# Kernel optimization log

Hardware: AMD Instinct MI355X
Metric: run time of the kernel (lower is better)

Reference implementation:

```python
import jax, jax.numpy as jnp
import numpy as np

NUM_HEADS = 12


def setup_inputs() -> dict:
    key = jax.random.key(0)
    k1, k2, k3, k4 = jax.random.split(key, 4)
    dim = 768
    B, N1, N2 = 8, 64, 4096  # N1 must equal head_dim = dim // num_heads
    x = jax.random.normal(k1, (B, N1, dim), dtype=jnp.float32)
    y = jax.random.normal(k2, (B, N2, dim), dtype=jnp.float32)
    # torch nn.Linear layout: [out_features, in_features]
    W_qkv = jax.random.normal(k3, (3 * dim, dim), dtype=jnp.float32) * 0.02
    W_proj = jax.random.normal(k4, (dim, dim), dtype=jnp.float32) * 0.02
    b_proj = jnp.zeros((dim,), dtype=jnp.float32)
    return {"x": x, "y": y, "W_qkv": W_qkv, "W_proj": W_proj, "b_proj": b_proj}


def _split_heads(t, H):
    # [B, N, C] -> [B, H, N, C//H]
    B, N, C = t.shape
    return t.reshape(B, N, H, C // H).transpose(0, 2, 1, 3)


def reference(x, y, W_qkv, W_proj, b_proj):
    H = NUM_HEADS
    B1, N1, C = x.shape
    B2, N2, _ = y.shape
    hd = C // H
    scale = hd ** -0.5

    # qkv projections (bias=False); take q from x, k/v from y
    qkv_x = x @ W_qkv.T                      # [B, N1, 3C]
    q = _split_heads(qkv_x[..., :C], H)      # [B, H, N1, hd]
    qkv_y = y @ W_qkv.T                      # [B, N2, 3C]
    k = _split_heads(qkv_y[..., C:2 * C], H)  # [B, H, N2, hd]
    v = _split_heads(qkv_y[..., 2 * C:], H)   # [B, H, N2, hd]

    attn = jnp.einsum('bhqd,bhkd->bhqk', q, k) * scale  # [B, H, N1, N2]
    attn = jax.nn.softmax(attn, axis=-1)
    attn_t = attn.transpose(0, 1, 3, 2)       # [B, H, N2, N1]; N1 == hd

    # non-standard elementwise combine with v (requires N1 == hd)
    out = attn_t * v                          # [B, H, N2, hd]
    out = out.transpose(0, 2, 1, 3).reshape(B2, N2, C)
    return out @ W_proj.T + b_proj
```

## Files before the change

### kernel.cpp

```cpp
#include <hip/hip_runtime.h>
#include <math.h>


typedef __attribute__((ext_vector_type(8))) short short8;
typedef __attribute__((ext_vector_type(4))) float f32x4;

__device__ __forceinline__ ushort f2bf(float x) {
  unsigned u = __float_as_uint(x);
  u += 0x7fffu + ((u >> 16) & 1u);
  return (ushort)(u >> 16);
}
__device__ __forceinline__ float bf2f(ushort h) {
  return __uint_as_float((unsigned)h << 16);
}

__device__ __forceinline__ void gl_lds16(const ushort* g, ushort* l) {
  __builtin_amdgcn_global_load_lds(
      (__attribute__((address_space(1))) void*)g,
      (__attribute__((address_space(3))) void*)l, 16, 0, 0);
}

__global__ __launch_bounds__(256) void cast_f32_bf16(
    const float* __restrict__ src, ushort* __restrict__ dst, int n) {
  int i = (blockIdx.x * 256 + threadIdx.x) * 8;
  if (i >= n) return;
  float4 a = *(const float4*)(src + i);
  float4 b = *(const float4*)(src + i + 4);
  ushort o[8] = {f2bf(a.x), f2bf(a.y), f2bf(a.z), f2bf(a.w),
                 f2bf(b.x), f2bf(b.y), f2bf(b.z), f2bf(b.w)};
  *(uint4*)(dst + i) = *(const uint4*)o;
}

template <typename CT>
__global__ __launch_bounds__(256) void gemm_bf16_nt(
    const ushort* __restrict__ A, int lda,
    const ushort* __restrict__ B, int ldb,
    CT* __restrict__ C, int ldc, int K,
    const float* __restrict__ bias,
    int m_tiles, int n_tiles, int swz)
{
  __shared__ __align__(16) ushort As[2][4096];
  __shared__ __align__(16) ushort Bs[2][4096];
  const int tid = threadIdx.x;
  int rt, ct;
  {
    int id = blockIdx.x;
    if (swz) {
      int xcd = id & 7, local = id >> 3;
      int per = n_tiles * 16;
      int grp = local / per, s = local % per;
      rt = xcd * (m_tiles >> 3) + grp * 16 + (s & 15);
      ct = s >> 4;
    } else { rt = id % m_tiles; ct = id / m_tiles; }
  }
  const int m0 = rt * 128, n0 = ct * 128;

  const int w = tid >> 6, lane = tid & 63;
  const int lm = lane & 15, quad = lane >> 4;
  const int wm = (w & 1) * 64, wn = (w >> 1) * 64;

  const int G0 = w * 64 + lane, G1 = G0 + 256;
  const int r0 = G0 >> 2, c0 = ((G0 & 3) - (r0 >> 1)) & 3;
  const int r1 = G1 >> 2, c1 = ((G1 & 3) - (r1 >> 1)) & 3;
  const ushort* Ag0 = A + (size_t)(m0 + r0) * lda + c0 * 8;
  const ushort* Ag1 = A + (size_t)(m0 + r1) * lda + c1 * 8;
  const ushort* Bg0 = B + (size_t)(n0 + r0) * ldb + c0 * 8;
  const ushort* Bg1 = B + (size_t)(n0 + r1) * ldb + c1 * 8;
  const int lds0 = w * 512, lds1 = w * 512 + 2048;

  f32x4 acc[4][4];
#pragma unroll
  for (int i = 0; i < 4; ++i)
#pragma unroll
    for (int j = 0; j < 4; ++j) acc[i][j] = (f32x4)(0.f);

  const int nk = K >> 5;
  gl_lds16(Ag0, &As[0][lds0]); gl_lds16(Ag1, &As[0][lds1]);
  gl_lds16(Bg0, &Bs[0][lds0]); gl_lds16(Bg1, &Bs[0][lds1]);

  int cur = 0;
  for (int kk = 0; kk < nk; ++kk) {
    __syncthreads();
    if (kk + 1 < nk) {
      const int k0 = (kk + 1) << 5;
      gl_lds16(Ag0 + k0, &As[cur ^ 1][lds0]); gl_lds16(Ag1 + k0, &As[cur ^ 1][lds1]);
      gl_lds16(Bg0 + k0, &Bs[cur ^ 1][lds0]); gl_lds16(Bg1 + k0, &Bs[cur ^ 1][lds1]);
    }
    const ushort* Ab = &As[cur][0];
    const ushort* Bb = &Bs[cur][0];
    short8 af[4], bf8[4];
#pragma unroll
    for (int i = 0; i < 4; ++i) {
      const int Ra = wm + i * 16 + lm;
      af[i] = *(const short8*)(const void*)(Ab + Ra * 32 + ((quad + (Ra >> 1)) & 3) * 8);
      const int Rb = wn + i * 16 + lm;
      bf8[i] = *(const short8*)(const void*)(Bb + Rb * 32 + ((quad + (Rb >> 1)) & 3) * 8);
    }
#pragma unroll
    for (int i = 0; i < 4; ++i)
#pragma unroll
      for (int j = 0; j < 4; ++j)
        acc[i][j] = __builtin_amdgcn_mfma_f32_16x16x32_bf16(af[i], bf8[j], acc[i][j], 0, 0, 0);
    cur ^= 1;
  }
  __syncthreads();

  if constexpr (sizeof(CT) == 2) {
    ushort* eb = ((ushort*)&Bs[0][0]) + w * 2048;
#pragma unroll
    for (int i = 0; i < 4; ++i) {
      ushort* ebc = eb + (i & 1) * 1024;
#pragma unroll
      for (int j = 0; j < 4; ++j)
#pragma unroll
        for (int r = 0; r < 4; ++r) {
          const int R = quad * 4 + r;
          const int gt = j * 2 + (lm >> 3);
          const int gs = (gt + R) & 7;
          ebc[R * 64 + gs * 8 + (lm & 7)] = f2bf(acc[i][j][r]);
        }
#pragma unroll
      for (int p = 0; p < 2; ++p) {
        const int R2 = (lane >> 3) + p * 8;
        const int g = lane & 7;
        const int gt2 = (g - R2) & 7;
        uint4 v = *(const uint4*)(const void*)(ebc + R2 * 64 + g * 8);
        *(uint4*)(C + (size_t)(m0 + wm + i * 16 + R2) * ldc + n0 + wn + gt2 * 8) = v;
      }
    }
  } else {
#pragma unroll
    for (int j = 0; j < 4; ++j) {
      const int col = n0 + wn + j * 16 + lm;
      const float bb = bias ? bias[col] : 0.f;
#pragma unroll
      for (int i = 0; i < 4; ++i) {
        const int row = m0 + wm + i * 16 + quad * 4;
#pragma unroll
        for (int r = 0; r < 4; ++r)
          C[(size_t)(row + r) * ldc + col] = (CT)(acc[i][j][r] + bb);
      }
    }
  }
}

__global__ __launch_bounds__(256) void attn_pass1(
    const ushort* __restrict__ Q,
    const ushort* __restrict__ KV,
    float* __restrict__ parts)
{
  const int chunk = blockIdx.x, h = blockIdx.y, b = blockIdx.z;
  const int tid = threadIdx.x;
  __shared__ __align__(16) ushort Qs[64 * 72];
  __shared__ __align__(16) ushort Ks[128 * 72];
  __shared__ float sm[4][64], ss[4][64];
#pragma unroll
  for (int p = 0; p < 2; ++p) {
    const int G = tid + 256 * p, row = G >> 3, g = G & 7;
    *(uint4*)(Qs + row * 72 + g * 8) =
        *(const uint4*)(Q + (size_t)(b * 64 + row) * 768 + h * 64 + g * 8);
  }
#pragma unroll
  for (int p = 0; p < 4; ++p) {
    const int G = tid + 256 * p, row = G >> 3, g = G & 7;
    *(uint4*)(Ks + row * 72 + g * 8) =
        *(const uint4*)(KV + (size_t)(b * 4096 + chunk * 128 + row) * 1536 + h * 64 + g * 8);
  }
  __syncthreads();

  const int w = tid >> 6, lane = tid & 63;
  const int lm = lane & 15, quad = lane >> 4;
  const int wn = w * 32;

  f32x4 acc[4][2];
#pragma unroll
  for (int i = 0; i < 4; ++i) { acc[i][0] = (f32x4)(0.f); acc[i][1] = (f32x4)(0.f); }
#pragma unroll
  for (int s = 0; s < 2; ++s) {
    short8 qf[4], kf[2];
#pragma unroll
    for (int i = 0; i < 4; ++i)
      qf[i] = *(const short8*)(const void*)(Qs + (i * 16 + lm) * 72 + s * 32 + quad * 8);
#pragma unroll
    for (int jn = 0; jn < 2; ++jn)
      kf[jn] = *(const short8*)(const void*)(Ks + (wn + jn * 16 + lm) * 72 + s * 32 + quad * 8);
#pragma unroll
    for (int i = 0; i < 4; ++i)
#pragma unroll
      for (int jn = 0; jn < 2; ++jn)
        acc[i][jn] = __builtin_amdgcn_mfma_f32_16x16x32_bf16(qf[i], kf[jn], acc[i][jn], 0, 0, 0);
  }

#pragma unroll
  for (int i = 0; i < 4; ++i)
#pragma unroll
    for (int r = 0; r < 4; ++r) {
      float v0 = acc[i][0][r] * 0.125f, v1 = acc[i][1][r] * 0.125f;
      float m = fmaxf(v0, v1);
      m = fmaxf(m, __shfl_xor(m, 1)); m = fmaxf(m, __shfl_xor(m, 2));
      m = fmaxf(m, __shfl_xor(m, 4)); m = fmaxf(m, __shfl_xor(m, 8));
      float e = __expf(v0 - m) + __expf(v1 - m);
      e += __shfl_xor(e, 1); e += __shfl_xor(e, 2);
      e += __shfl_xor(e, 4); e += __shfl_xor(e, 8);
      if (lm == 0) {
        const int j = i * 16 + quad * 4 + r;
        sm[w][j] = m; ss[w][j] = e;
      }
    }
  __syncthreads();
  if (tid < 64) {
    float g = fmaxf(fmaxf(sm[0][tid], sm[1][tid]), fmaxf(sm[2][tid], sm[3][tid]));
    float s = ss[0][tid] * __expf(sm[0][tid] - g) + ss[1][tid] * __expf(sm[1][tid] - g)
            + ss[2][tid] * __expf(sm[2][tid] - g) + ss[3][tid] * __expf(sm[3][tid] - g);
    const int bh = b * 12 + h;
    float* p = parts + ((size_t)(bh * 32 + chunk) * 64 + tid) * 2;
    p[0] = g; p[1] = s;
  }
}

__global__ void attn_combine(const float* __restrict__ parts, float* __restrict__ stats)
{
  const int bh = blockIdx.x, j = threadIdx.x;
  float pm[32], ps[32];
  float g = -1e30f;
#pragma unroll
  for (int c = 0; c < 32; ++c) {
    const float* p = parts + ((size_t)(bh * 32 + c) * 64 + j) * 2;
    pm[c] = p[0]; ps[c] = p[1];
    g = fmaxf(g, pm[c]);
  }
  float s = 0.f;
#pragma unroll
  for (int c = 0; c < 32; ++c) s += ps[c] * __expf(pm[c] - g);
  stats[(size_t)(bh * 64 + j) * 2]     = g;
  stats[(size_t)(bh * 64 + j) * 2 + 1] = 1.f / s;
}

__global__ __launch_bounds__(256) void attn_pass2(
    const ushort* __restrict__ Q, const ushort* __restrict__ KV,
    const float* __restrict__ stats, ushort* __restrict__ E)
{
  const int chunk = blockIdx.x, h = blockIdx.y, b = blockIdx.z;
  const int tid = threadIdx.x;
  __shared__ __align__(16) ushort Qs[64 * 72];
  __shared__ __align__(16) ushort Ks[128 * 72];
  __shared__ __align__(16) ushort Vs[128 * 72];
  __shared__ float st[64][2];
#pragma unroll
  for (int p = 0; p < 2; ++p) {
    const int G = tid + 256 * p, row = G >> 3, g = G & 7;
    *(uint4*)(Qs + row * 72 + g * 8) =
        *(const uint4*)(Q + (size_t)(b * 64 + row) * 768 + h * 64 + g * 8);
  }
#pragma unroll
  for (int p = 0; p < 4; ++p) {
    const int G = tid + 256 * p, row = G >> 3, g = G & 7;
    const size_t rbase = (size_t)(b * 4096 + chunk * 128 + row) * 1536 + h * 64 + g * 8;
    *(uint4*)(Ks + row * 72 + g * 8) = *(const uint4*)(KV + rbase);
    *(uint4*)(Vs + row * 72 + g * 8) = *(const uint4*)(KV + rbase + 768);
  }
  const int bh = b * 12 + h;
  if (tid < 128) st[tid >> 1][tid & 1] = stats[(size_t)(bh * 64 + (tid >> 1)) * 2 + (tid & 1)];
  __syncthreads();

  const int w = tid >> 6, lane = tid & 63;
  const int lm = lane & 15, quad = lane >> 4;
  const int wn = w * 32;

  f32x4 acc[4][2];
#pragma unroll
  for (int i = 0; i < 4; ++i) { acc[i][0] = (f32x4)(0.f); acc[i][1] = (f32x4)(0.f); }
#pragma unroll
  for (int s = 0; s < 2; ++s) {
    short8 qf[4], kf[2];
#pragma unroll
    for (int i = 0; i < 4; ++i)
      qf[i] = *(const short8*)(const void*)(Qs + (i * 16 + lm) * 72 + s * 32 + quad * 8);
#pragma unroll
    for (int jn = 0; jn < 2; ++jn)
      kf[jn] = *(const short8*)(const void*)(Ks + (wn + jn * 16 + lm) * 72 + s * 32 + quad * 8);
#pragma unroll
    for (int i = 0; i < 4; ++i)
#pragma unroll
      for (int jn = 0; jn < 2; ++jn)
        acc[i][jn] = __builtin_amdgcn_mfma_f32_16x16x32_bf16(qf[i], kf[jn], acc[i][jn], 0, 0, 0);
  }

  ushort ev[4][2][4];
#pragma unroll
  for (int i = 0; i < 4; ++i)
#pragma unroll
    for (int jn = 0; jn < 2; ++jn)
#pragma unroll
      for (int r = 0; r < 4; ++r) {
        const float v = acc[i][jn][r] * 0.125f;
        const int j = i * 16 + quad * 4 + r;
        const float p = __expf(v - st[j][0]) * st[j][1];
        const int key = wn + jn * 16 + lm;
        ev[i][jn][r] = f2bf(p * bf2f(Vs[key * 72 + j]));
      }
  __syncthreads();
  ushort* Es = Ks;
#pragma unroll
  for (int i = 0; i < 4; ++i)
#pragma unroll
    for (int jn = 0; jn < 2; ++jn)
#pragma unroll
      for (int r = 0; r < 4; ++r)
        Es[(wn + jn * 16 + lm) * 72 + i * 16 + quad * 4 + r] = ev[i][jn][r];
  __syncthreads();
#pragma unroll
  for (int k = 0; k < 4; ++k) {
    const int row = tid >> 1, g = (tid & 1) * 4 + k;
    uint4 v = *(const uint4*)(const void*)(Es + row * 72 + g * 8);
    *(uint4*)(E + (size_t)(b * 4096 + chunk * 128 + row) * 768 + h * 64 + g * 8) = v;
  }
}

extern "C" void kernel_launch(void* const* d_in, const int* in_sizes, int n_in,
                              void* d_out, int out_size, void* d_ws, size_t ws_size,
                              hipStream_t stream) {
  const float* x     = (const float*)d_in[0];
  const float* y     = (const float*)d_in[1];
  const float* Wqkv  = (const float*)d_in[2];
  const float* Wproj = (const float*)d_in[3];
  const float* bproj = (const float*)d_in[4];
  float* out = (float*)d_out;

  char* wsb = (char*)d_ws;
  ushort* xbf    = (ushort*)(wsb + 0);
  ushort* qbf    = (ushort*)(wsb + 786432);
  ushort* wqkvbf = (ushort*)(wsb + 1572864);
  float*  parts  = (float*)(wsb + 1572864);
  float*  stats  = (float*)(wsb + 3145728);
  ushort* wpbf   = (ushort*)(wsb + 5111808);
  ushort* ybf    = (ushort*)(wsb + 6291456);
  ushort* Ebf    = ybf;
  ushort* KVbf   = (ushort*)(wsb + 56623104);

  cast_f32_bf16<<<(393216/8 + 255)/256, 256, 0, stream>>>(x, xbf, 393216);
  cast_f32_bf16<<<(1769472/8 + 255)/256, 256, 0, stream>>>(Wqkv, wqkvbf, 1769472);
  cast_f32_bf16<<<(589824/8 + 255)/256, 256, 0, stream>>>(Wproj, wpbf, 589824);
  cast_f32_bf16<<<(25165824/8 + 255)/256, 256, 0, stream>>>(y, ybf, 25165824);

  gemm_bf16_nt<ushort><<<24, 256, 0, stream>>>(
      xbf, 768, wqkvbf, 768, qbf, 768, 768, nullptr, 4, 6, 0);
  gemm_bf16_nt<ushort><<<3072, 256, 0, stream>>>(
      ybf, 768, wqkvbf + (size_t)768 * 768, 768, KVbf, 1536, 768, nullptr, 256, 12, 1);

  attn_pass1<<<dim3(32, 12, 8), 256, 0, stream>>>(qbf, KVbf, parts);
  attn_combine<<<96, 64, 0, stream>>>(parts, stats);
  attn_pass2<<<dim3(32, 12, 8), 256, 0, stream>>>(qbf, KVbf, stats, Ebf);

  gemm_bf16_nt<float><<<1536, 256, 0, stream>>>(
      Ebf, 768, wpbf, 768, out, 768, 768, bproj, 256, 6, 1);
}
```

Before: 418.3 us.

## Merge casts and QKV GEMMs, triple-buffer GEMM, fold softmax combine into pass2

Merges the four cast launches into one kernel and the Q and KV projection GEMMs into a single launch. Folds the softmax statistic combine into attn_pass2, so each block reduces the per-chunk partials itself. The GEMM mainloop moves from double to triple buffering with explicit vmcnt waits and raw barriers, so loads run two stages ahead. This cuts launch count and adds memory-latency hiding, at the cost of more LDS per block and redundant combine work in every pass2 block.

New measurement: 405.4 us. -3.1%, faster.

```diff
diff --git a/kernel.cpp b/kernel.cpp
--- a/kernel.cpp
+++ b/kernel.cpp
@@ -20,39 +20,35 @@
       (__attribute__((address_space(3))) void*)l, 16, 0, 0);
 }
 
-__global__ __launch_bounds__(256) void cast_f32_bf16(
-    const float* __restrict__ src, ushort* __restrict__ dst, int n) {
-  int i = (blockIdx.x * 256 + threadIdx.x) * 8;
-  if (i >= n) return;
-  float4 a = *(const float4*)(src + i);
-  float4 b = *(const float4*)(src + i + 4);
+__global__ __launch_bounds__(256) void cast_all(
+    const float* __restrict__ x, ushort* __restrict__ xb,
+    const float* __restrict__ w1, ushort* __restrict__ w1b,
+    const float* __restrict__ w2, ushort* __restrict__ w2b,
+    const float* __restrict__ y, ushort* __restrict__ yb) {
+  long i = (long)(blockIdx.x * 256 + threadIdx.x) * 8;
+  if (i >= 27918336L) return;
+  const float* s; ushort* d; long off;
+  if (i < 393216L)        { s = x;  d = xb;  off = i; }
+  else if (i < 2162688L)  { s = w1; d = w1b; off = i - 393216L; }
+  else if (i < 2752512L)  { s = w2; d = w2b; off = i - 2162688L; }
+  else                    { s = y;  d = yb;  off = i - 2752512L; }
+  float4 a = *(const float4*)(s + off);
+  float4 b = *(const float4*)(s + off + 4);
   ushort o[8] = {f2bf(a.x), f2bf(a.y), f2bf(a.z), f2bf(a.w),
                  f2bf(b.x), f2bf(b.y), f2bf(b.z), f2bf(b.w)};
-  *(uint4*)(dst + i) = *(const uint4*)o;
+  *(uint4*)(d + off) = *(const uint4*)o;
 }
 
 template <typename CT>
-__global__ __launch_bounds__(256) void gemm_bf16_nt(
+__device__ __forceinline__ void gemm_body(
     const ushort* __restrict__ A, int lda,
     const ushort* __restrict__ B, int ldb,
     CT* __restrict__ C, int ldc, int K,
-    const float* __restrict__ bias,
-    int m_tiles, int n_tiles, int swz)
-{
-  __shared__ __align__(16) ushort As[2][4096];
-  __shared__ __align__(16) ushort Bs[2][4096];
+    const float* __restrict__ bias, int rt, int ct)
+{
+  __shared__ __align__(16) ushort As[3][4096];
+  __shared__ __align__(16) ushort Bs[3][4096];
   const int tid = threadIdx.x;
-  int rt, ct;
-  {
-    int id = blockIdx.x;
-    if (swz) {
-      int xcd = id & 7, local = id >> 3;
-      int per = n_tiles * 16;
-      int grp = local / per, s = local % per;
-      rt = xcd * (m_tiles >> 3) + grp * 16 + (s & 15);
-      ct = s >> 4;
-    } else { rt = id % m_tiles; ct = id / m_tiles; }
-  }
   const int m0 = rt * 128, n0 = ct * 128;
 
   const int w = tid >> 6, lane = tid & 63;
@@ -77,17 +73,22 @@
   const int nk = K >> 5;
   gl_lds16(Ag0, &As[0][lds0]); gl_lds16(Ag1, &As[0][lds1]);
   gl_lds16(Bg0, &Bs[0][lds0]); gl_lds16(Bg1, &Bs[0][lds1]);
-
-  int cur = 0;
+  gl_lds16(Ag0 + 32, &As[1][lds0]); gl_lds16(Ag1 + 32, &As[1][lds1]);
+  gl_lds16(Bg0 + 32, &Bs[1][lds0]); gl_lds16(Bg1 + 32, &Bs[1][lds1]);
+  asm volatile("s_waitcnt vmcnt(4)" ::: "memory");
+
   for (int kk = 0; kk < nk; ++kk) {
-    __syncthreads();
-    if (kk + 1 < nk) {
-      const int k0 = (kk + 1) << 5;
-      gl_lds16(Ag0 + k0, &As[cur ^ 1][lds0]); gl_lds16(Ag1 + k0, &As[cur ^ 1][lds1]);
-      gl_lds16(Bg0 + k0, &Bs[cur ^ 1][lds0]); gl_lds16(Bg1 + k0, &Bs[cur ^ 1][lds1]);
-    }
-    const ushort* Ab = &As[cur][0];
-    const ushort* Bb = &Bs[cur][0];
+    __builtin_amdgcn_s_barrier();
+    __builtin_amdgcn_sched_barrier(0);
+    if (kk + 2 < nk) {
+      const int k0 = (kk + 2) << 5;
+      ushort* Ad = &As[(kk + 2) % 3][0];
+      ushort* Bd = &Bs[(kk + 2) % 3][0];
+      gl_lds16(Ag0 + k0, Ad + lds0); gl_lds16(Ag1 + k0, Ad + lds1);
+      gl_lds16(Bg0 + k0, Bd + lds0); gl_lds16(Bg1 + k0, Bd + lds1);
+    }
+    const ushort* Ab = &As[kk % 3][0];
+    const ushort* Bb = &Bs[kk % 3][0];
     short8 af[4], bf8[4];
 #pragma unroll
     for (int i = 0; i < 4; ++i) {
@@ -101,7 +102,8 @@
 #pragma unroll
       for (int j = 0; j < 4; ++j)
         acc[i][j] = __builtin_amdgcn_mfma_f32_16x16x32_bf16(af[i], bf8[j], acc[i][j], 0, 0, 0);
-    cur ^= 1;
+    if (kk < nk - 2)       asm volatile("s_waitcnt vmcnt(4)" ::: "memory");
+    else if (kk == nk - 2) asm volatile("s_waitcnt vmcnt(0)" ::: "memory");
   }
   __syncthreads();
 
@@ -142,6 +144,41 @@
       }
     }
   }
+}
+
+__global__ __launch_bounds__(256) void qkv_gemm(
+    const ushort* __restrict__ xbf, const ushort* __restrict__ ybf,
+    const ushort* __restrict__ wqkv, ushort* __restrict__ qbf,
+    ushort* __restrict__ kvbf)
+{
+  const int id = blockIdx.x;
+  const ushort *A, *B; ushort* C; int ldc, rt, ct;
+  if (id < 3072) {
+    const int xcd = id & 7, local = id >> 3;
+    const int per = 12 * 16;
+    const int grp = local / per, s = local % per;
+    rt = xcd * 32 + grp * 16 + (s & 15);
+    ct = s >> 4;
+    A = ybf; B = wqkv + (size_t)768 * 768; C = kvbf; ldc = 1536;
+  } else {
+    const int id2 = id - 3072;
+    rt = id2 & 3; ct = id2 >> 2;
+    A = xbf; B = wqkv; C = qbf; ldc = 768;
+  }
+  gemm_body<ushort>(A, 768, B, 768, C, ldc, 768, nullptr, rt, ct);
+}
+
+__global__ __launch_bounds__(256) void out_gemm(
+    const ushort* __restrict__ Ebf, const ushort* __restrict__ wpbf,
+    const float* __restrict__ bias, float* __restrict__ out)
+{
+  const int id = blockIdx.x;
+  const int xcd = id & 7, local = id >> 3;
+  const int per = 6 * 16;
+  const int grp = local / per, s = local % per;
+  const int rt = xcd * 32 + grp * 16 + (s & 15);
+  const int ct = s >> 4;
+  gemm_body<float>(Ebf, 768, wpbf, 768, out, 768, 768, bias, rt, ct);
 }
 
 __global__ __launch_bounds__(256) void attn_pass1(
@@ -218,27 +255,9 @@
   }
 }
 
-__global__ void attn_combine(const float* __restrict__ parts, float* __restrict__ stats)
-{
-  const int bh = blockIdx.x, j = threadIdx.x;
-  float pm[32], ps[32];
-  float g = -1e30f;
-#pragma unroll
-  for (int c = 0; c < 32; ++c) {
-    const float* p = parts + ((size_t)(bh * 32 + c) * 64 + j) * 2;
-    pm[c] = p[0]; ps[c] = p[1];
-    g = fmaxf(g, pm[c]);
-  }
-  float s = 0.f;
-#pragma unroll
-  for (int c = 0; c < 32; ++c) s += ps[c] * __expf(pm[c] - g);
-  stats[(size_t)(bh * 64 + j) * 2]     = g;
-  stats[(size_t)(bh * 64 + j) * 2 + 1] = 1.f / s;
-}
-
 __global__ __launch_bounds__(256) void attn_pass2(
     const ushort* __restrict__ Q, const ushort* __restrict__ KV,
-    const float* __restrict__ stats, ushort* __restrict__ E)
+    const float* __restrict__ parts, ushort* __restrict__ E)
 {
   const int chunk = blockIdx.x, h = blockIdx.y, b = blockIdx.z;
   const int tid = threadIdx.x;
@@ -259,8 +278,26 @@
     *(uint4*)(Ks + row * 72 + g * 8) = *(const uint4*)(KV + rbase);
     *(uint4*)(Vs + row * 72 + g * 8) = *(const uint4*)(KV + rbase + 768);
   }
-  const int bh = b * 12 + h;
-  if (tid < 128) st[tid >> 1][tid & 1] = stats[(size_t)(bh * 64 + (tid >> 1)) * 2 + (tid & 1)];
+  {
+    const int bh = b * 12 + h;
+    const int tq = tid >> 2, tc = tid & 3;
+    float pm[8], ps[8];
+    float gm = -1e30f;
+#pragma unroll
+    for (int c = 0; c < 8; ++c) {
+      const float* p = parts + ((size_t)(bh * 32 + tc * 8 + c) * 64 + tq) * 2;
+      pm[c] = p[0]; ps[c] = p[1];
+      gm = fmaxf(gm, pm[c]);
+    }
+    gm = fmaxf(gm, __shfl_xor(gm, 1));
+    gm = fmaxf(gm, __shfl_xor(gm, 2));
+    float s = 0.f;
+#pragma unroll
+    for (int c = 0; c < 8; ++c) s += ps[c] * __expf(pm[c] - gm);
+    s += __shfl_xor(s, 1);
+    s += __shfl_xor(s, 2);
+    if (tc == 0) { st[tq][0] = gm; st[tq][1] = 1.f / s; }
+  }
   __syncthreads();
 
   const int w = tid >> 6, lane = tid & 63;
@@ -332,26 +369,17 @@
   ushort* qbf    = (ushort*)(wsb + 786432);
   ushort* wqkvbf = (ushort*)(wsb + 1572864);
   float*  parts  = (float*)(wsb + 1572864);
-  float*  stats  = (float*)(wsb + 3145728);
   ushort* wpbf   = (ushort*)(wsb + 5111808);
   ushort* ybf    = (ushort*)(wsb + 6291456);
   ushort* Ebf    = ybf;
   ushort* KVbf   = (ushort*)(wsb + 56623104);
 
-  cast_f32_bf16<<<(393216/8 + 255)/256, 256, 0, stream>>>(x, xbf, 393216);
-  cast_f32_bf16<<<(1769472/8 + 255)/256, 256, 0, stream>>>(Wqkv, wqkvbf, 1769472);
-  cast_f32_bf16<<<(589824/8 + 255)/256, 256, 0, stream>>>(Wproj, wpbf, 589824);
-  cast_f32_bf16<<<(25165824/8 + 255)/256, 256, 0, stream>>>(y, ybf, 25165824);
-
-  gemm_bf16_nt<ushort><<<24, 256, 0, stream>>>(
-      xbf, 768, wqkvbf, 768, qbf, 768, 768, nullptr, 4, 6, 0);
-  gemm_bf16_nt<ushort><<<3072, 256, 0, stream>>>(
-      ybf, 768, wqkvbf + (size_t)768 * 768, 768, KVbf, 1536, 768, nullptr, 256, 12, 1);
+  cast_all<<<13632, 256, 0, stream>>>(x, xbf, Wqkv, wqkvbf, Wproj, wpbf, y, ybf);
+
+  qkv_gemm<<<3096, 256, 0, stream>>>(xbf, ybf, wqkvbf, qbf, KVbf);
 
   attn_pass1<<<dim3(32, 12, 8), 256, 0, stream>>>(qbf, KVbf, parts);
-  attn_combine<<<96, 64, 0, stream>>>(parts, stats);
-  attn_pass2<<<dim3(32, 12, 8), 256, 0, stream>>>(qbf, KVbf, stats, Ebf);
-
-  gemm_bf16_nt<float><<<1536, 256, 0, stream>>>(
-      Ebf, 768, wpbf, 768, out, 768, 768, bproj, 256, 6, 1);
-}
+  attn_pass2<<<dim3(32, 12, 8), 256, 0, stream>>>(qbf, KVbf, parts, Ebf);
+
+  out_gemm<<<1536, 256, 0, stream>>>(Ebf, wpbf, bproj, out);
+}
```
